# Performance work log

Hardware: AMD Instinct MI355X
Metric: run time of the kernel (lower is better)

The kernel has to match this reference:

```python
import jax, jax.numpy as jnp
import numpy as np
import math

B, T, D, H = 2, 2048, 768, 12
ND = D // H  # head dim = 64


def precompute_freqs_cis(dim, end, theta=10000.0):
    freqs = 1.0 / (theta ** (jnp.arange(0, dim, 2, dtype=jnp.float32) / dim))  # [dim/2]
    t = jnp.arange(end, dtype=jnp.float32)
    freqs = jnp.outer(t, freqs)  # [end, dim/2]
    return jnp.cos(freqs), jnp.sin(freqs)


def apply_rotary_emb(q, k, cos, sin):
    # q, k: [b, t, h, nd]; cos/sin: [t, nd/2]
    def rot(x):
        xr, xi = x[..., 0::2], x[..., 1::2]  # even/odd interleaved split
        c = cos[None, :, None, :]
        s = sin[None, :, None, :]
        out_r = xr * c - xi * s
        out_i = xr * s + xi * c
        return jnp.stack([out_r, out_i], axis=-1).reshape(x.shape)
    return rot(q), rot(k)


def setup_inputs() -> dict:
    key = jax.random.key(0)
    ks = jax.random.split(key, 12)
    sc = 0.02
    q = jax.random.normal(ks[0], (B, T, D), dtype=jnp.float32)
    k = jax.random.normal(ks[1], (B, T, D), dtype=jnp.float32)
    v = jax.random.normal(ks[2], (B, T, D), dtype=jnp.float32)
    mask = jnp.tril(jnp.ones((T, T), dtype=jnp.int32))[None, None]  # causal [1,1,T,T]
    # weights stored as [d_in, d_out] (pre-transposed vs torch Linear)
    wq = jax.random.normal(ks[3], (D, D), dtype=jnp.float32) * sc
    bq = jax.random.normal(ks[4], (D,), dtype=jnp.float32) * sc
    wk = jax.random.normal(ks[5], (D, D), dtype=jnp.float32) * sc
    bk = jax.random.normal(ks[6], (D,), dtype=jnp.float32) * sc
    wv = jax.random.normal(ks[7], (D, D), dtype=jnp.float32) * sc
    bv = jax.random.normal(ks[8], (D,), dtype=jnp.float32) * sc
    wo = jax.random.normal(ks[9], (D, D), dtype=jnp.float32) * sc
    cos, sin = precompute_freqs_cis(ND, T)
    return {"q": q, "k": k, "v": v, "mask": mask, "wq": wq, "bq": bq,
            "wk": wk, "bk": bk, "wv": wv, "bv": bv, "wo": wo,
            "freqs_cos": cos, "freqs_sin": sin}


def reference(q, k, v, mask, wq, bq, wk, bk, wv, bv, wo, freqs_cos, freqs_sin):
    b, t, d = q.shape
    qh = (q @ wq + bq).reshape(b, t, H, ND)
    kh = (k @ wk + bk).reshape(b, t, H, ND)
    vh = (v @ wv + bv).reshape(b, t, H, ND).transpose(0, 2, 1, 3)  # [b,h,t,nd]
    qh, kh = apply_rotary_emb(qh, kh, freqs_cos[:t], freqs_sin[:t])
    qh = qh.transpose(0, 2, 1, 3)  # [b,h,t,nd]
    kh = kh.transpose(0, 2, 1, 3)
    attn = jnp.einsum('bhqd,bhkd->bhqk', qh, kh) / math.sqrt(ND)
    attn = jnp.where(mask == 0, jnp.float32(-jnp.inf), attn)
    probs = jax.nn.softmax(attn, axis=-1)
    out = jnp.einsum('bhqk,bhkd->bhqd', probs, vh)
    out = out.transpose(0, 2, 1, 3).reshape(b, t, d)
    return out @ wo
```

## Files before the change

kernel.cpp:

```cpp
#include <hip/hip_runtime.h>
#include <hip/hip_bf16.h>
#include <math.h>

#define BB 2
#define TT 2048
#define DD 768
#define HH 12
#define ND 64
#define MM (BB*TT)

typedef __attribute__((ext_vector_type(8))) short bf16x8;
typedef __attribute__((ext_vector_type(4))) float f32x4;
typedef __attribute__((ext_vector_type(16))) float f32x16;

__device__ __forceinline__ float bf2f(ushort u) {
    union { unsigned int i; float f; } v; v.i = ((unsigned int)u) << 16; return v.f;
}
__device__ __forceinline__ ushort f2bf(float f) {
    union { float f; unsigned int i; } v; v.f = f;
    unsigned int r = v.i + 0x7FFF + ((v.i >> 16) & 1);
    return (ushort)(r >> 16);
}

__device__ __forceinline__ void cp16(void* lds, const void* g) {
    __builtin_amdgcn_global_load_lds(
        (const __attribute__((address_space(1))) void*)g,
        (__attribute__((address_space(3))) void*)lds, 16, 0, 0);
}

__device__ __forceinline__ float fexp2(float x) {
    float r; asm("v_exp_f32 %0, %1" : "=v"(r) : "v"(x)); return r;
}
__device__ __forceinline__ unsigned int pk_bf16(float a, float b) {
    unsigned int r; asm("v_cvt_pk_bf16_f32 %0, %1, %2" : "=v"(r) : "v"(a), "v"(b)); return r;
}

__device__ __forceinline__ void plswap(unsigned int& a, unsigned int& b) {
#if __has_builtin(__builtin_amdgcn_permlane32_swap)
    auto r = __builtin_amdgcn_permlane32_swap(a, b, false, false);
    a = r[0]; b = r[1];
#else
    unsigned int sa = __shfl_xor((int)a, 32), sb = __shfl_xor((int)b, 32);
    bool hi = (threadIdx.x & 63) >= 32;
    unsigned int na = hi ? sb : a, nb = hi ? b : sa;
    a = na; b = nb;
#endif
}
__device__ __forceinline__ float partner32(float x, int hi) {
#if __has_builtin(__builtin_amdgcn_permlane32_swap)
    unsigned int u = __float_as_uint(x);
    auto r = __builtin_amdgcn_permlane32_swap(u, u, false, false);
    return __uint_as_float(hi ? r[0] : r[1]);
#else
    return __shfl_xor(x, 32);
#endif
}

#define QSCALE 0.18033688011112043f

__global__ __launch_bounds__(256) void conv_all(
    const float* __restrict__ x0, const float* __restrict__ x1, const float* __restrict__ x2,
    ushort* __restrict__ o0, ushort* __restrict__ o1, ushort* __restrict__ o2,
    const float* __restrict__ w0, const float* __restrict__ w1,
    const float* __restrict__ w2, const float* __restrict__ w3,
    ushort* __restrict__ t0, ushort* __restrict__ t1,
    ushort* __restrict__ t2, ushort* __restrict__ t3)
{
    const int z = blockIdx.z;
    if (z < 3) {
        const float* x = z == 0 ? x0 : (z == 1 ? x1 : x2);
        ushort* o = z == 0 ? o0 : (z == 1 ? o1 : o2);
        const int total4 = MM * DD / 4;
        for (int i = blockIdx.x * 256 + threadIdx.x; i < total4; i += gridDim.x * 256) {
            float4 v = *(const float4*)&x[i * 4];
            ushort4 r;
            r.x = f2bf(v.x); r.y = f2bf(v.y); r.z = f2bf(v.z); r.w = f2bf(v.w);
            *(ushort4*)&o[i * 4] = r;
        }
    } else {
        if (blockIdx.x >= (DD / 64) * (DD / 64)) return;
        __shared__ ushort tile[64][72];
        const int zz = z - 3;
        const float* w = zz == 0 ? w0 : zz == 1 ? w1 : zz == 2 ? w2 : w3;
        ushort* o = zz == 0 ? t0 : zz == 1 ? t1 : zz == 2 ? t2 : t3;
        const int n0 = (blockIdx.x % (DD / 64)) * 64;
        const int k0 = (blockIdx.x / (DD / 64)) * 64;
        #pragma unroll
        for (int it = 0; it < 4; ++it) {
            int e = (threadIdx.x + it * 256) * 4;
            int r = e >> 6, c = e & 63;
            float4 v = *(const float4*)&w[(size_t)(k0 + r) * DD + n0 + c];
            tile[c + 0][r] = f2bf(v.x);
            tile[c + 1][r] = f2bf(v.y);
            tile[c + 2][r] = f2bf(v.z);
            tile[c + 3][r] = f2bf(v.w);
        }
        __syncthreads();
        #pragma unroll
        for (int it = 0; it < 4; ++it) {
            int e = (threadIdx.x + it * 256) * 4;
            int nr = e >> 6, kc = e & 63;
            ushort4 r4;
            r4.x = tile[nr][kc + 0];
            r4.y = tile[nr][kc + 1];
            r4.z = tile[nr][kc + 2];
            r4.w = tile[nr][kc + 3];
            *(ushort4*)&o[(size_t)(n0 + nr) * DD + k0 + kc] = r4;
        }
    }
}

struct GArgs { const ushort* x; const ushort* wt; const float* bias; void* out;
               const float* cT; const float* sT; int rope; };

template<int MODE, int TM, int TN>
__global__ __launch_bounds__(256) void gemm_bf16(GArgs a0, GArgs a1, GArgs a2)
{
    constexpr int WM = TM / 2, WN = TN / 2;
    constexpr int MF = WM / 16, NF = WN / 16;
    constexpr int ABYTES = TM * 128;
    constexpr int BUFB = (TM + TN) * 128;
    constexpr int NPASS = BUFB / 4096;
    constexpr int NK = DD / 64;
    __shared__ __align__(16) ushort S[2][BUFB / 2];
    GArgs ga = (blockIdx.z == 0) ? a0 : (blockIdx.z == 1 ? a1 : a2);
    const int tid = threadIdx.x;
    const int w = tid >> 6, l = tid & 63;
    const int wr = w >> 1, wc = w & 1;
    const int n0 = blockIdx.x * TN, m0 = blockIdx.y * TM;

    f32x4 acc[MF][NF] = {};

    auto stage = [&](int buf, int k0) {
        #pragma unroll
        for (int it = 0; it < NPASS; ++it) {
            const int ob = it * 4096 + w * 1024;
            const int o = ob + l * 16;
            if (ob < ABYTES) {
                const int row = o >> 7, inner = o & 127;
                cp16((char*)&S[buf][0] + ob,
                     (const char*)ga.x + (size_t)(m0 + row) * (DD * 2) + k0 * 2 +
                     (inner ^ ((row & 7) << 4)));
            } else {
                const int o2 = o - ABYTES;
                const int row = o2 >> 7, inner = o2 & 127;
                cp16((char*)&S[buf][0] + ob,
                     (const char*)ga.wt + (size_t)(n0 + row) * (DD * 2) + k0 * 2 +
                     (inner ^ ((row & 7) << 4)));
            }
        }
    };

    stage(0, 0);
    __syncthreads();
    const int lq = l >> 4, lr = l & 15;
    for (int t = 0; t < NK; ++t) {
        const int cur = t & 1;
        if (t + 1 < NK) stage(cur ^ 1, (t + 1) * 64);
        const char* ab = (const char*)&S[cur][0];
        #pragma unroll
        for (int kc = 0; kc < 2; ++kc) {
            const int kb = kc * 64 + lq * 16;
            bf16x8 af[MF], bfr[NF];
            #pragma unroll
            for (int i = 0; i < MF; ++i) {
                const int row = WM * wr + 16 * i + lr;
                af[i] = *(const bf16x8*)(ab + row * 128 + (kb ^ ((row & 7) << 4)));
            }
            #pragma unroll
            for (int j = 0; j < NF; ++j) {
                const int row = WN * wc + 16 * j + lr;
                bfr[j] = *(const bf16x8*)(ab + ABYTES + row * 128 + (kb ^ ((row & 7) << 4)));
            }
            __builtin_amdgcn_s_setprio(1);
            #pragma unroll
            for (int i = 0; i < MF; ++i)
                #pragma unroll
                for (int j = 0; j < NF; ++j)
                    acc[i][j] = __builtin_amdgcn_mfma_f32_16x16x32_bf16(af[i], bfr[j], acc[i][j], 0, 0, 0);
            __builtin_amdgcn_s_setprio(0);
        }
        __syncthreads();
    }

    if (MODE == 0 && ga.rope == -1) {
        ushort* tl = (ushort*)&S[0][0];
        #pragma unroll
        for (int i = 0; i < MF; ++i) {
            #pragma unroll
            for (int j = 0; j < NF; ++j) {
                #pragma unroll
                for (int r = 0; r < 4; ++r) {
                    const int ml = WM * wr + 16 * i + (l >> 4) * 4 + r;
                    const int nl = WN * wc + 16 * j + (l & 15);
                    tl[nl * (TM + 8) + ml] = f2bf(acc[i][j][r] + ga.bias[n0 + nl]);
                }
            }
        }
        __syncthreads();
        const int b = m0 >> 11, t0b = m0 & 2047;
        ushort* base = (ushort*)ga.out + ((size_t)(b * DD + n0)) * TT + t0b;
        #pragma unroll
        for (int it = 0; it < TM * TN / (256 * 8); ++it) {
            const int slot = tid + it * 256;
            const int d = slot / (TM / 8), c = (slot % (TM / 8)) * 8;
            bf16x8 v = *(const bf16x8*)&tl[d * (TM + 8) + c];
            *(bf16x8*)&base[(size_t)d * TT + c] = v;
        }
        return;
    }

    #pragma unroll
    for (int i = 0; i < MF; ++i) {
        #pragma unroll
        for (int j = 0; j < NF; ++j) {
            #pragma unroll
            for (int r = 0; r < 4; ++r) {
                const int m = m0 + WM * wr + 16 * i + (l >> 4) * 4 + r;
                const int n = n0 + WN * wc + 16 * j + (l & 15);
                float v = acc[i][j][r];
                if (MODE == 0) {
                    v += ga.bias[n];
                    const int tt = m & 2047;
                    if (ga.rope > 0) {
                        const int d = n & 63;
                        const float c = ga.cT[tt * 32 + (d >> 1)];
                        const float s = ga.sT[tt * 32 + (d >> 1)];
                        const float pv = __shfl_xor(v, 1);
                        v = (n & 1) ? (pv * s + v * c) : (v * c - pv * s);
                        if (ga.rope == 2) v *= QSCALE;
                    }
                    const int b = m >> 11;
                    const int h = n >> 6, d = n & 63;
                    ((ushort*)ga.out)[((size_t)(b * HH + h) * TT + tt) * ND + d] = f2bf(v);
                } else {
                    ((float*)ga.out)[(size_t)m * DD + n] = v;
                }
            }
        }
    }
}

#define NQB (TT/128)
#define NBH (BB*HH)
#define NTASK (NQB*NBH)
#define NCU 256

__global__ __launch_bounds__(512) void attn_mfma4(const ushort* __restrict__ Qh,
                                                  const ushort* __restrict__ Kh,
                                                  const ushort* __restrict__ VhT,
                                                  ushort* __restrict__ Op)
{
    __shared__ __align__(16) ushort Ks[2][2][4096];
    __shared__ __align__(16) ushort Vs[2][2][4096];
    const int tid = threadIdx.x;
    const int w = tid >> 6, l = tid & 63;
    const int lq = l & 31, hi = l >> 5;
    const int qs = w & 3;
    const int kvh = w >> 2;

    const int n = blockIdx.x;
    const int r_ = (n < NCU) ? n : (NTASK - 1 + NCU - n);
    const int qblk = (NQB - 1) - r_ / NBH;
    const int bh = r_ % NBH;

    const int q0 = qblk * 128;
    const int q0w = q0 + qs * 32;
    const int qg = q0w + lq;
    const int ntH = qblk + 1;
    const int kvbase = kvh * ntH * 64;

    const ushort* Qg = Qh + ((size_t)bh * TT + q0w) * ND;
    const ushort* Kg = Kh + (size_t)bh * TT * ND;
    const ushort* Vg = VhT + (size_t)bh * ND * TT;

    bf16x8 qf[4];
    #pragma unroll
    for (int ks = 0; ks < 4; ++ks)
        qf[ks] = *(const bf16x8*)((const char*)Qg + lq * 128 + ks * 32 + hi * 16);

    auto stageKV = [&](int buf, int kv0) {
        #pragma unroll
        for (int it = 0; it < 2; ++it) {
            int o = it * 4096 + qs * 1024 + l * 16;
            int row = o >> 7, inner = o & 127;
            int swz = inner ^ ((row & 7) << 4);
            cp16((char*)&Ks[kvh][buf][0] + it * 4096 + qs * 1024,
                 (const char*)Kg + (size_t)(kv0 + row) * 128 + swz);
            cp16((char*)&Vs[kvh][buf][0] + it * 4096 + qs * 1024,
                 (const char*)Vg + (size_t)row * (TT * 2) + kv0 * 2 + swz);
        }
    };

    float m = -1e30f, lsum = 0.f;
    f32x16 o0 = {}, o1 = {};

    stageKV(0, kvbase);
    __syncthreads();
    for (int t = 0; t < ntH; ++t) {
        const int cur = t & 1;
        if (t + 1 < ntH) stageKV(cur ^ 1, kvbase + (t + 1) * 64);
        const char* kb = (const char*)&Ks[kvh][cur][0];
        const char* vb = (const char*)&Vs[kvh][cur][0];
        const int kvt = kvbase + t * 64;

        if (kvt <= q0w + 31) {
            const bool have1 = (kvt + 32 <= q0w + 31);

            f32x16 st0 = {}, st1 = {};
            __builtin_amdgcn_s_setprio(1);
            #pragma unroll
            for (int ks = 0; ks < 4; ++ks) {
                bf16x8 kf = *(const bf16x8*)(kb + lq * 128 +
                                             ((ks * 32 + hi * 16) ^ ((lq & 7) << 4)));
                st0 = __builtin_amdgcn_mfma_f32_32x32x16_bf16(kf, qf[ks], st0, 0, 0, 0);
            }
            if (have1) {
                #pragma unroll
                for (int ks = 0; ks < 4; ++ks) {
                    bf16x8 kf = *(const bf16x8*)(kb + (32 + lq) * 128 +
                                                 ((ks * 32 + hi * 16) ^ ((lq & 7) << 4)));
                    st1 = __builtin_amdgcn_mfma_f32_32x32x16_bf16(kf, qf[ks], st1, 0, 0, 0);
                }
            }
            __builtin_amdgcn_s_setprio(0);

            float tm = -1e30f;
            if (kvt + 31 > q0w) {
                #pragma unroll
                for (int r = 0; r < 16; ++r) {
                    const int kvg = kvt + (r & 3) + 8 * (r >> 2) + 4 * hi;
                    float x = (kvg <= qg) ? st0[r] : -1e30f;
                    st0[r] = x;
                    tm = fmaxf(tm, x);
                }
            } else {
                #pragma unroll
                for (int r = 0; r < 16; ++r) tm = fmaxf(tm, st0[r]);
            }
            if (have1) {
                if (kvt + 63 > q0w) {
                    #pragma unroll
                    for (int r = 0; r < 16; ++r) {
                        const int kvg = kvt + 32 + (r & 3) + 8 * (r >> 2) + 4 * hi;
                        float x = (kvg <= qg) ? st1[r] : -1e30f;
                        st1[r] = x;
                        tm = fmaxf(tm, x);
                    }
                } else {
                    #pragma unroll
                    for (int r = 0; r < 16; ++r) tm = fmaxf(tm, st1[r]);
                }
            }
            tm = fmaxf(tm, partner32(tm, hi));

            const bool defer = __all(tm <= m + 11.5f);
            float alpha = 1.f;
            if (!defer) {
                const float nm = fmaxf(m, tm);
                alpha = fexp2(m - nm);
                m = nm;
            }

            float ps[16];
            unsigned int pkA[8], pkB[8];
            #pragma unroll
            for (int i = 0; i < 8; ++i) {
                const float p0 = fexp2(st0[2 * i + 0] - m);
                const float p1 = fexp2(st0[2 * i + 1] - m);
                pkA[i] = pk_bf16(p0, p1);
                ps[i] = p0 + p1;
            }
            if (have1) {
                #pragma unroll
                for (int i = 0; i < 8; ++i) {
                    const float p0 = fexp2(st1[2 * i + 0] - m);
                    const float p1 = fexp2(st1[2 * i + 1] - m);
                    pkB[i] = pk_bf16(p0, p1);
                    ps[8 + i] = p0 + p1;
                }
            } else {
                #pragma unroll
                for (int i = 0; i < 8; ++i) { pkB[i] = 0; ps[8 + i] = 0.f; }
            }
            const float t0s = (ps[0] + ps[1]) + (ps[2] + ps[3]);
            const float t1s = (ps[4] + ps[5]) + (ps[6] + ps[7]);
            const float t2s = (ps[8] + ps[9]) + (ps[10] + ps[11]);
            const float t3s = (ps[12] + ps[13]) + (ps[14] + ps[15]);
            float rs = (t0s + t1s) + (t2s + t3s);
            rs += partner32(rs, hi);
            lsum = lsum * alpha + rs;

            plswap(pkA[0], pkA[2]); plswap(pkA[1], pkA[3]);
            plswap(pkA[4], pkA[6]); plswap(pkA[5], pkA[7]);
            if (have1) {
                plswap(pkB[0], pkB[2]); plswap(pkB[1], pkB[3]);
                plswap(pkB[4], pkB[6]); plswap(pkB[5], pkB[7]);
            }
            union { unsigned int u[4]; bf16x8 v; } pa0, pa1, pa2, pa3;
            pa0.u[0] = pkA[0]; pa0.u[1] = pkA[1]; pa0.u[2] = pkA[2]; pa0.u[3] = pkA[3];
            pa1.u[0] = pkA[4]; pa1.u[1] = pkA[5]; pa1.u[2] = pkA[6]; pa1.u[3] = pkA[7];
            pa2.u[0] = pkB[0]; pa2.u[1] = pkB[1]; pa2.u[2] = pkB[2]; pa2.u[3] = pkB[3];
            pa3.u[0] = pkB[4]; pa3.u[1] = pkB[5]; pa3.u[2] = pkB[6]; pa3.u[3] = pkB[7];

            if (!defer) {
                #pragma unroll
                for (int r = 0; r < 16; ++r) { o0[r] *= alpha; o1[r] *= alpha; }
            }

            __builtin_amdgcn_s_setprio(1);
            #pragma unroll
            for (int sl = 0; sl < 2; ++sl) {
                const bf16x8 pf = sl == 0 ? pa0.v : pa1.v;
                const int cb = sl * 32 + hi * 16;
                bf16x8 va = *(const bf16x8*)(vb + lq * 128 + (cb ^ ((lq & 7) << 4)));
                bf16x8 vc = *(const bf16x8*)(vb + (lq + 32) * 128 + (cb ^ ((lq & 7) << 4)));
                o0 = __builtin_amdgcn_mfma_f32_32x32x16_bf16(va, pf, o0, 0, 0, 0);
                o1 = __builtin_amdgcn_mfma_f32_32x32x16_bf16(vc, pf, o1, 0, 0, 0);
            }
            if (have1) {
                #pragma unroll
                for (int sl = 0; sl < 2; ++sl) {
                    const bf16x8 pf = sl == 0 ? pa2.v : pa3.v;
                    const int cb = 64 + sl * 32 + hi * 16;
                    bf16x8 va = *(const bf16x8*)(vb + lq * 128 + (cb ^ ((lq & 7) << 4)));
                    bf16x8 vc = *(const bf16x8*)(vb + (lq + 32) * 128 + (cb ^ ((lq & 7) << 4)));
                    o0 = __builtin_amdgcn_mfma_f32_32x32x16_bf16(va, pf, o0, 0, 0, 0);
                    o1 = __builtin_amdgcn_mfma_f32_32x32x16_bf16(vc, pf, o1, 0, 0, 0);
                }
            }
            __builtin_amdgcn_s_setprio(0);
        }
        __syncthreads();
    }

    float* xO  = (float*)&Ks[0][0][0];
    float* xML = (float*)&Vs[0][0][0];
    if (kvh == 1) {
        float* dst = xO + qs * 2048;
        #pragma unroll
        for (int r = 0; r < 16; ++r) {
            dst[r * 64 + l] = o0[r];
            dst[(r + 16) * 64 + l] = o1[r];
        }
        if (hi == 0) { xML[qs * 64 + lq] = m; xML[qs * 64 + 32 + lq] = lsum; }
    }
    __syncthreads();
    if (kvh == 0) {
        const float* src = xO + qs * 2048;
        const float m1 = xML[qs * 64 + lq];
        const float l1 = xML[qs * 64 + 32 + lq];
        const float ms = fmaxf(m, m1);
        const float a0 = fexp2(m - ms), a1 = fexp2(m1 - ms);
        const float inv = 1.0f / (lsum * a0 + l1 * a1);
        const int b = bh / HH, h = bh % HH;
        ushort* dst = Op + ((size_t)(b * TT + qg)) * DD + h * ND;
        #pragma unroll
        for (int g = 0; g < 4; ++g) {
            ushort4 w0, w1;
            w0.x = f2bf((o0[4 * g + 0] * a0 + src[(4 * g + 0) * 64 + l] * a1) * inv);
            w0.y = f2bf((o0[4 * g + 1] * a0 + src[(4 * g + 1) * 64 + l] * a1) * inv);
            w0.z = f2bf((o0[4 * g + 2] * a0 + src[(4 * g + 2) * 64 + l] * a1) * inv);
            w0.w = f2bf((o0[4 * g + 3] * a0 + src[(4 * g + 3) * 64 + l] * a1) * inv);
            *(ushort4*)&dst[8 * g + 4 * hi] = w0;
            w1.x = f2bf((o1[4 * g + 0] * a0 + src[(16 + 4 * g + 0) * 64 + l] * a1) * inv);
            w1.y = f2bf((o1[4 * g + 1] * a0 + src[(16 + 4 * g + 1) * 64 + l] * a1) * inv);
            w1.z = f2bf((o1[4 * g + 2] * a0 + src[(16 + 4 * g + 2) * 64 + l] * a1) * inv);
            w1.w = f2bf((o1[4 * g + 3] * a0 + src[(16 + 4 * g + 3) * 64 + l] * a1) * inv);
            *(ushort4*)&dst[32 + 8 * g + 4 * hi] = w1;
        }
    }
}

extern "C" void kernel_launch(void* const* d_in, const int* in_sizes, int n_in,
                              void* d_out, int out_size, void* d_ws, size_t ws_size,
                              hipStream_t stream)
{
    const float* q  = (const float*)d_in[0];
    const float* k  = (const float*)d_in[1];
    const float* v  = (const float*)d_in[2];
    const float* wq = (const float*)d_in[4];
    const float* bq = (const float*)d_in[5];
    const float* wk = (const float*)d_in[6];
    const float* bk = (const float*)d_in[7];
    const float* wv = (const float*)d_in[8];
    const float* bv = (const float*)d_in[9];
    const float* wo = (const float*)d_in[10];
    const float* fc = (const float*)d_in[11];
    const float* fs = (const float*)d_in[12];
    float* out = (float*)d_out;

    ushort* qB  = (ushort*)d_ws;
    ushort* kB  = qB  + (size_t)MM * DD;
    ushort* vB  = kB  + (size_t)MM * DD;
    ushort* wqT = vB  + (size_t)MM * DD;
    ushort* wkT = wqT + (size_t)DD * DD;
    ushort* wvT = wkT + (size_t)DD * DD;
    ushort* woT = wvT + (size_t)DD * DD;
    ushort* Qh  = woT + (size_t)DD * DD;
    ushort* Kh  = Qh  + (size_t)MM * DD;
    ushort* VhT = Kh  + (size_t)MM * DD;
    ushort* Op  = qB;

    conv_all<<<dim3(2048, 1, 7), 256, 0, stream>>>(q, k, v, qB, kB, vB,
                                                   wq, wk, wv, wo, wqT, wkT, wvT, woT);

    GArgs aq{qB, wqT, bq, (void*)Qh, fc, fs, 2};
    GArgs ak{kB, wkT, bk, (void*)Kh, fc, fs, 1};
    GArgs av{vB, wvT, bv, (void*)VhT, nullptr, nullptr, -1};
    gemm_bf16<0, 128, 96><<<dim3(DD / 96, MM / 128, 3), 256, 0, stream>>>(aq, ak, av);

    attn_mfma4<<<dim3(NTASK), 512, 0, stream>>>(Qh, Kh, VhT, Op);

    GArgs ao{Op, woT, nullptr, (void*)out, nullptr, nullptr, 0};
    gemm_bf16<1, 128, 96><<<dim3(DD / 96, MM / 128, 1), 256, 0, stream>>>(ao, ao, ao);
}
```

Before: 104.6 us.

## Flatten GEMM grids with XCD-aware block remap and smaller tiles; compact conv grid

The GEMM kernels now take a flat 1D grid and remap block ids so consecutive tasks land on the same XCD (interleaved by 8). Tile sizes shrink (128x64 for QKV, 64x64 for the output projection), raising the block count to fill more CUs. The conversion kernel's grid is repacked so the weight-transpose tiles are spread across the z-slices, removing idle blocks. Smaller tiles reduce data reuse per block, and the remap assumes the block count divides evenly by 8.

```diff
diff --git a/kernel.cpp b/kernel.cpp
--- a/kernel.cpp
+++ b/kernel.cpp
@@ -67,24 +67,25 @@
     ushort* __restrict__ t2, ushort* __restrict__ t3)
 {
     const int z = blockIdx.z;
-    if (z < 3) {
+    if (blockIdx.x < 2048) {
         const float* x = z == 0 ? x0 : (z == 1 ? x1 : x2);
         ushort* o = z == 0 ? o0 : (z == 1 ? o1 : o2);
         const int total4 = MM * DD / 4;
-        for (int i = blockIdx.x * 256 + threadIdx.x; i < total4; i += gridDim.x * 256) {
+        for (int i = blockIdx.x * 256 + threadIdx.x; i < total4; i += 2048 * 256) {
             float4 v = *(const float4*)&x[i * 4];
             ushort4 r;
             r.x = f2bf(v.x); r.y = f2bf(v.y); r.z = f2bf(v.z); r.w = f2bf(v.w);
             *(ushort4*)&o[i * 4] = r;
         }
     } else {
-        if (blockIdx.x >= (DD / 64) * (DD / 64)) return;
         __shared__ ushort tile[64][72];
-        const int zz = z - 3;
+        const int widx = z * 192 + (blockIdx.x - 2048);
+        const int zz = widx / 144;
+        const int tl = widx % 144;
         const float* w = zz == 0 ? w0 : zz == 1 ? w1 : zz == 2 ? w2 : w3;
         ushort* o = zz == 0 ? t0 : zz == 1 ? t1 : zz == 2 ? t2 : t3;
-        const int n0 = (blockIdx.x % (DD / 64)) * 64;
-        const int k0 = (blockIdx.x / (DD / 64)) * 64;
+        const int n0 = (tl % (DD / 64)) * 64;
+        const int k0 = (tl / (DD / 64)) * 64;
         #pragma unroll
         for (int it = 0; it < 4; ++it) {
             int e = (threadIdx.x + it * 256) * 4;
@@ -114,7 +115,8 @@
                const float* cT; const float* sT; int rope; };
 
 template<int MODE, int TM, int TN>
-__global__ __launch_bounds__(256) void gemm_bf16(GArgs a0, GArgs a1, GArgs a2)
+__global__ __launch_bounds__(256) void gemm_bf16(GArgs a0, GArgs a1, GArgs a2,
+                                                 int nx, int ny)
 {
     constexpr int WM = TM / 2, WN = TN / 2;
     constexpr int MF = WM / 16, NF = WN / 16;
@@ -123,11 +125,18 @@
     constexpr int NPASS = BUFB / 4096;
     constexpr int NK = DD / 64;
     __shared__ __align__(16) ushort S[2][BUFB / 2];
-    GArgs ga = (blockIdx.z == 0) ? a0 : (blockIdx.z == 1 ? a1 : a2);
     const int tid = threadIdx.x;
     const int w = tid >> 6, l = tid & 63;
     const int wr = w >> 1, wc = w & 1;
-    const int n0 = blockIdx.x * TN, m0 = blockIdx.y * TM;
+
+    const int per = gridDim.x >> 3;
+    const int p = blockIdx.x;
+    const int task = (p & 7) * per + (p >> 3);
+    const int bx = task % nx;
+    const int by = (task / nx) % ny;
+    const int bz = task / (nx * ny);
+    GArgs ga = (bz == 0) ? a0 : (bz == 1 ? a1 : a2);
+    const int n0 = bx * TN, m0 = by * TM;
 
     f32x4 acc[MF][NF] = {};
 
@@ -502,16 +511,16 @@
     ushort* VhT = Kh  + (size_t)MM * DD;
     ushort* Op  = qB;
 
-    conv_all<<<dim3(2048, 1, 7), 256, 0, stream>>>(q, k, v, qB, kB, vB,
+    conv_all<<<dim3(2240, 1, 3), 256, 0, stream>>>(q, k, v, qB, kB, vB,
                                                    wq, wk, wv, wo, wqT, wkT, wvT, woT);
 
     GArgs aq{qB, wqT, bq, (void*)Qh, fc, fs, 2};
     GArgs ak{kB, wkT, bk, (void*)Kh, fc, fs, 1};
     GArgs av{vB, wvT, bv, (void*)VhT, nullptr, nullptr, -1};
-    gemm_bf16<0, 128, 96><<<dim3(DD / 96, MM / 128, 3), 256, 0, stream>>>(aq, ak, av);
+    gemm_bf16<0, 128, 64><<<dim3(1152), 256, 0, stream>>>(aq, ak, av, DD / 64, MM / 128);
 
     attn_mfma4<<<dim3(NTASK), 512, 0, stream>>>(Qh, Kh, VhT, Op);
 
     GArgs ao{Op, woT, nullptr, (void*)out, nullptr, nullptr, 0};
-    gemm_bf16<1, 128, 96><<<dim3(DD / 96, MM / 128, 1), 256, 0, stream>>>(ao, ao, ao);
-}
+    gemm_bf16<1, 64, 64><<<dim3(768), 256, 0, stream>>>(ao, ao, ao, DD / 64, MM / 64);
+}
```

New measurement: 95.56 us. 1.09x faster.
